# Kernel tuning notes

Measured on AMD Instinct MI355X. Metric: run time of the kernel, lower is better.

## Reference

```python
import jax, jax.numpy as jnp
import numpy as np

H = 128

def _rnn_layer(inp, W_ih, W_hh, b_ih, b_hh):
    # inp: [B, T, D]; precompute the input projection for all timesteps at once
    pre = jnp.einsum('btd,hd->bth', inp, W_ih) + b_ih + b_hh  # [B, T, H]
    B = inp.shape[0]
    h0 = jnp.zeros((B, H), dtype=inp.dtype)

    def step(h, p_t):  # p_t: [B, H]
        h_new = jnp.tanh(p_t + h @ W_hh.T)
        return h_new, h_new

    _, hs = jax.lax.scan(step, h0, jnp.swapaxes(pre, 0, 1))  # [T, B, H]
    return jnp.swapaxes(hs, 0, 1)  # [B, T, H]


def setup_inputs() -> dict:
    key = jax.random.key(0)
    ks = jax.random.split(key, 12)
    B, T, D = 64, 512, 2048
    s_in = 1.0 / np.sqrt(H)  # PyTorch RNN init scale ~ U(-1/sqrt(H), 1/sqrt(H))
    u = lambda k, shape: jax.random.uniform(k, shape, jnp.float32, -s_in, s_in)
    return {
        'x': jax.random.normal(ks[0], (B, T, D), jnp.float32),
        'W_ih1': u(ks[1], (H, D)),
        'W_hh1': u(ks[2], (H, H)),
        'b_ih1': u(ks[3], (H,)),
        'b_hh1': u(ks[4], (H,)),
        'W_ih2': u(ks[5], (H, H)),
        'W_hh2': u(ks[6], (H, H)),
        'b_ih2': u(ks[7], (H,)),
        'b_hh2': u(ks[8], (H,)),
        'W_fc': u(ks[9], (1, H)),
        'b_fc': u(ks[10], (1,)),
    }


def reference(x, W_ih1, W_hh1, b_ih1, b_hh1, W_ih2, W_hh2, b_ih2, b_hh2, W_fc, b_fc):
    h1 = _rnn_layer(x, W_ih1, W_hh1, b_ih1, b_hh1)   # [B, T, H]
    h2 = _rnn_layer(h1, W_ih2, W_hh2, b_ih2, b_hh2)  # [B, T, H]
    last = h2[:, -1, :]                               # [B, H]
    return last @ W_fc.T + b_fc                       # [B, 1]
```

## Files before the change

### kernel.cpp

```cpp
#include <hip/hip_runtime.h>
#include <cstddef>

#define BB 64
#define TT 512
#define DD 2048
#define HH 128
#define M1 (BB*TT)

__device__ __forceinline__ float tanh_fast(float x) {
    float e2x = __builtin_amdgcn_exp2f(x * 2.885390081777927f);
    return 1.0f - 2.0f * __builtin_amdgcn_rcpf(e2x + 1.0f);
}

template<int K>
__global__ __launch_bounds__(256) void gemm_bias_kernel(
    const float* __restrict__ A, const float* __restrict__ W,
    const float* __restrict__ bia, const float* __restrict__ bib,
    float* __restrict__ out)
{
    constexpr int BM = 64, BK = 16;
    constexpr int NK = K / BK;
    __shared__ float As[BK][68];
    __shared__ float Bs[BK][132];

    const int tid = threadIdx.x;
    const int tc = tid & 15;
    const int tr = tid >> 4;
    const size_t m0 = (size_t)blockIdx.x * BM;

    const int arow = tid >> 2;
    const int ak4  = (tid & 3) * 4;
    const int bn0  = tid >> 1;
    const int bk   = (tid & 1) * 8;

    const float* Aptr = A + (m0 + arow) * (size_t)K + ak4;
    const float* Wptr = W + (size_t)bn0 * K + bk;

    float4 ra  = *(const float4*)Aptr;
    float4 rb0 = *(const float4*)(Wptr);
    float4 rb1 = *(const float4*)(Wptr + 4);

    float acc[4][8];
#pragma unroll
    for (int i = 0; i < 4; i++)
#pragma unroll
        for (int j = 0; j < 8; j++) acc[i][j] = 0.0f;

    for (int kt = 0; kt < NK; ++kt) {
        __syncthreads();
        As[ak4 + 0][arow] = ra.x;
        As[ak4 + 1][arow] = ra.y;
        As[ak4 + 2][arow] = ra.z;
        As[ak4 + 3][arow] = ra.w;
        Bs[bk + 0][bn0] = rb0.x;
        Bs[bk + 1][bn0] = rb0.y;
        Bs[bk + 2][bn0] = rb0.z;
        Bs[bk + 3][bn0] = rb0.w;
        Bs[bk + 4][bn0] = rb1.x;
        Bs[bk + 5][bn0] = rb1.y;
        Bs[bk + 6][bn0] = rb1.z;
        Bs[bk + 7][bn0] = rb1.w;
        __syncthreads();
        if (kt + 1 < NK) {
            ra  = *(const float4*)(Aptr + (size_t)(kt + 1) * BK);
            rb0 = *(const float4*)(Wptr + (size_t)(kt + 1) * BK);
            rb1 = *(const float4*)(Wptr + (size_t)(kt + 1) * BK + 4);
        }
#pragma unroll
        for (int kk = 0; kk < BK; ++kk) {
            const float4 av = *(const float4*)&As[kk][tr * 4];
            const float4 b0 = *(const float4*)&Bs[kk][tc * 4];
            const float4 b1 = *(const float4*)&Bs[kk][64 + tc * 4];
            const float aa[4] = {av.x, av.y, av.z, av.w};
            const float bb[8] = {b0.x, b0.y, b0.z, b0.w, b1.x, b1.y, b1.z, b1.w};
#pragma unroll
            for (int i = 0; i < 4; i++)
#pragma unroll
                for (int j = 0; j < 8; j++)
                    acc[i][j] = __builtin_fmaf(aa[i], bb[j], acc[i][j]);
        }
    }

    float bs[8];
#pragma unroll
    for (int j = 0; j < 4; j++) {
        bs[j]     = bia[tc * 4 + j] + bib[tc * 4 + j];
        bs[j + 4] = bia[64 + tc * 4 + j] + bib[64 + tc * 4 + j];
    }
#pragma unroll
    for (int i = 0; i < 4; i++) {
        const size_t r = m0 + tr * 4 + i;
        float4 o0 = {acc[i][0] + bs[0], acc[i][1] + bs[1],
                     acc[i][2] + bs[2], acc[i][3] + bs[3]};
        float4 o1 = {acc[i][4] + bs[4], acc[i][5] + bs[5],
                     acc[i][6] + bs[6], acc[i][7] + bs[7]};
        *(float4*)&out[r * HH + tc * 4]      = o0;
        *(float4*)&out[r * HH + 64 + tc * 4] = o1;
    }
}

__global__ __launch_bounds__(512) void rnn_scan_kernel(
    const float* __restrict__ pre,
    const float* __restrict__ Whh,
    float* __restrict__ hout,
    const float* __restrict__ Wfc,
    const float* __restrict__ bfc,
    float* __restrict__ outv,
    const int store_h)
{
    __shared__ float hsh[2][160];
    __shared__ float wsum[8];

    const int tid  = threadIdx.x;
    const int wave = tid >> 6;
    const int lane = tid & 63;
    const int jj   = lane >> 3;
    const int kq   = lane & 7;
    const int j    = wave * 8 + jj;
    const int b    = blockIdx.x;


    float4 Wr0[4], Wr1[4];
    {
        const float* wp0 = Whh + (size_t)j * HH + kq * 16;
        const float* wp1 = Whh + (size_t)(j + 64) * HH + kq * 16;
#pragma unroll
        for (int q = 0; q < 4; q++) {
            Wr0[q] = *(const float4*)(wp0 + q * 4);
            Wr1[q] = *(const float4*)(wp1 + q * 4);
        }
    }

    if (tid < HH) hsh[0][(tid >> 4) * 20 + (tid & 15)] = 0.0f;
    __syncthreads();

    const float* pb = pre + (size_t)b * TT * HH;
    float pre_next0 = 0.f, pre_next1 = 0.f;
    if (kq == 0) { pre_next0 = pb[j]; pre_next1 = pb[j + 64]; }
    float hlast0 = 0.f, hlast1 = 0.f;

    for (int t = 0; t < TT; ++t) {
        const float* hr = hsh[t & 1];
        float* hw = hsh[(t + 1) & 1];
        const float pre_cur0 = pre_next0, pre_cur1 = pre_next1;
        if (kq == 0 && t + 1 < TT) {
            pre_next0 = pb[(size_t)(t + 1) * HH + j];
            pre_next1 = pb[(size_t)(t + 1) * HH + j + 64];
        }
        float acc0 = 0.f, acc1 = 0.f;
#pragma unroll
        for (int q = 0; q < 4; q++) {
            const float4 hv = *(const float4*)&hr[kq * 20 + q * 4];
            acc0 = __builtin_fmaf(Wr0[q].x, hv.x, acc0);
            acc0 = __builtin_fmaf(Wr0[q].y, hv.y, acc0);
            acc0 = __builtin_fmaf(Wr0[q].z, hv.z, acc0);
            acc0 = __builtin_fmaf(Wr0[q].w, hv.w, acc0);
            acc1 = __builtin_fmaf(Wr1[q].x, hv.x, acc1);
            acc1 = __builtin_fmaf(Wr1[q].y, hv.y, acc1);
            acc1 = __builtin_fmaf(Wr1[q].z, hv.z, acc1);
            acc1 = __builtin_fmaf(Wr1[q].w, hv.w, acc1);
        }
        acc0 += __shfl_xor(acc0, 1);  acc1 += __shfl_xor(acc1, 1);
        acc0 += __shfl_xor(acc0, 2);  acc1 += __shfl_xor(acc1, 2);
        acc0 += __shfl_xor(acc0, 4);  acc1 += __shfl_xor(acc1, 4);
        if (kq == 0) {
            const float h0 = tanh_fast(pre_cur0 + acc0);
            const float h1 = tanh_fast(pre_cur1 + acc1);
            hw[(j >> 4) * 20 + (j & 15)] = h0;
            hw[((j + 64) >> 4) * 20 + ((j + 64) & 15)] = h1;
            if (store_h) {
                hout[((size_t)b * TT + t) * HH + j]      = h0;
                hout[((size_t)b * TT + t) * HH + j + 64] = h1;
            }
            hlast0 = h0; hlast1 = h1;
        }
        __syncthreads();
    }

    if (!store_h) {
        float contrib = 0.f;
        if (kq == 0) contrib = hlast0 * Wfc[j] + hlast1 * Wfc[j + 64];
#pragma unroll
        for (int off = 1; off < 64; off <<= 1) contrib += __shfl_xor(contrib, off);
        if (lane == 0) wsum[wave] = contrib;
        __syncthreads();
        if (tid == 0) {
            float s = bfc[0];
#pragma unroll
            for (int w = 0; w < 8; w++) s += wsum[w];
            outv[b] = s;
        }
    }
}

extern "C" void kernel_launch(void* const* d_in, const int* in_sizes, int n_in,
                              void* d_out, int out_size, void* d_ws, size_t ws_size,
                              hipStream_t stream) {
    const float* x    = (const float*)d_in[0];
    const float* Wih1 = (const float*)d_in[1];
    const float* Whh1 = (const float*)d_in[2];
    const float* bih1 = (const float*)d_in[3];
    const float* bhh1 = (const float*)d_in[4];
    const float* Wih2 = (const float*)d_in[5];
    const float* Whh2 = (const float*)d_in[6];
    const float* bih2 = (const float*)d_in[7];
    const float* bhh2 = (const float*)d_in[8];
    const float* Wfc  = (const float*)d_in[9];
    const float* bfc  = (const float*)d_in[10];
    float* out = (float*)d_out;

    float* preA = (float*)d_ws;
    float* h1b  = preA + (size_t)M1 * HH;

    gemm_bias_kernel<DD><<<dim3(M1 / 64), dim3(256), 0, stream>>>(x, Wih1, bih1, bhh1, preA);
    rnn_scan_kernel<<<dim3(BB), dim3(512), 0, stream>>>(preA, Whh1, h1b, Wfc, bfc, out, 1);
    gemm_bias_kernel<HH><<<dim3(M1 / 64), dim3(256), 0, stream>>>(h1b, Wih2, bih2, bhh2, preA);
    rnn_scan_kernel<<<dim3(BB), dim3(512), 0, stream>>>(preA, Whh2, h1b, Wfc, bfc, out, 0);
}
```

Baseline: 940.5 us.

## Use f16 MFMA for input projections and f16 dot2 recurrent scan

Replaces the fp32 SIMT GEMMs with f16 MFMA 16x16x32 GEMMs, adding kernels that pre-convert the input weights to half precision. The recurrence scan drops from 512 to 128 threads, with each thread holding a full W_hh row in registers as packed halves and using fdot2, so the shuffle reduction goes away. The scan also prefetches 8 timesteps of pre-activations, and the hidden states passed to layer 2 are stored as f16 to halve that traffic. This targets both the GEMM compute cost and the per-step latency of the serial scan, at the cost of reduced precision.

```diff
diff --git a/kernel.cpp b/kernel.cpp
--- a/kernel.cpp
+++ b/kernel.cpp
@@ -1,5 +1,6 @@
 #include <hip/hip_runtime.h>
 #include <cstddef>
+#include <cstdint>
 
 #define BB 64
 #define TT 512
@@ -7,189 +8,171 @@
 #define HH 128
 #define M1 (BB*TT)
 
+typedef __attribute__((ext_vector_type(8))) _Float16 f16x8;
+typedef __attribute__((ext_vector_type(4))) float f32x4;
+typedef __attribute__((ext_vector_type(2))) _Float16 h2f;
+
 __device__ __forceinline__ float tanh_fast(float x) {
     float e2x = __builtin_amdgcn_exp2f(x * 2.885390081777927f);
     return 1.0f - 2.0f * __builtin_amdgcn_rcpf(e2x + 1.0f);
 }
-
-template<int K>
-__global__ __launch_bounds__(256) void gemm_bias_kernel(
-    const float* __restrict__ A, const float* __restrict__ W,
+__device__ __forceinline__ h2f bch2(unsigned u) { return __builtin_bit_cast(h2f, u); }
+
+__global__ __launch_bounds__(256) void prep_f16_kernel(
+    const float* __restrict__ W, _Float16* __restrict__ Wf)
+{
+    const int i = (blockIdx.x * 256 + threadIdx.x) * 4;
+    float4 w = *(const float4*)(W + i);
+    f16x8 dummy;
+    _Float16 o0 = (_Float16)w.x, o1 = (_Float16)w.y;
+    _Float16 o2 = (_Float16)w.z, o3 = (_Float16)w.w;
+    ushort4 ov;
+    ov.x = __builtin_bit_cast(unsigned short, o0);
+    ov.y = __builtin_bit_cast(unsigned short, o1);
+    ov.z = __builtin_bit_cast(unsigned short, o2);
+    ov.w = __builtin_bit_cast(unsigned short, o3);
+    *(ushort4*)((unsigned short*)Wf + i) = ov;
+    (void)dummy;
+}
+
+template<int K, bool CONVA>
+__global__ __launch_bounds__(256) void gemm_f16_mfma(
+    const void* __restrict__ Araw, const _Float16* __restrict__ Wf,
     const float* __restrict__ bia, const float* __restrict__ bib,
     float* __restrict__ out)
 {
-    constexpr int BM = 64, BK = 16;
-    constexpr int NK = K / BK;
-    __shared__ float As[BK][68];
-    __shared__ float Bs[BK][132];
-
-    const int tid = threadIdx.x;
-    const int tc = tid & 15;
-    const int tr = tid >> 4;
-    const size_t m0 = (size_t)blockIdx.x * BM;
-
-    const int arow = tid >> 2;
-    const int ak4  = (tid & 3) * 4;
-    const int bn0  = tid >> 1;
-    const int bk   = (tid & 1) * 8;
-
-    const float* Aptr = A + (m0 + arow) * (size_t)K + ak4;
-    const float* Wptr = W + (size_t)bn0 * K + bk;
-
-    float4 ra  = *(const float4*)Aptr;
-    float4 rb0 = *(const float4*)(Wptr);
-    float4 rb1 = *(const float4*)(Wptr + 4);
-
-    float acc[4][8];
-#pragma unroll
-    for (int i = 0; i < 4; i++)
-#pragma unroll
-        for (int j = 0; j < 8; j++) acc[i][j] = 0.0f;
+    constexpr int BK = 32, NK = K / BK;
+    __shared__ __align__(16) _Float16 Af[64 * 40];
+    __shared__ __align__(16) _Float16 Ws[128 * 40];
+
+    const int tid = threadIdx.x, wave = tid >> 6, lane = tid & 63;
+    const size_t m0 = (size_t)blockIdx.x * 64;
+    const int ar = tid >> 2, ak = (tid & 3) * 8;
+    const int wr = tid >> 1, wk = (tid & 1) * 16;
+    const _Float16* Wp = Wf + (size_t)wr * K + wk;
+    const int frow = lane & 15, fko = (lane >> 4) * 8;
+
+    f32x4 acc[8];
+#pragma unroll
+    for (int i = 0; i < 8; i++) acc[i] = (f32x4){0.f, 0.f, 0.f, 0.f};
 
     for (int kt = 0; kt < NK; ++kt) {
+        f16x8 astage;
+        if (CONVA) {
+            const float* Ap = (const float*)Araw + (m0 + ar) * (size_t)K + kt * BK + ak;
+            float4 a0 = *(const float4*)Ap;
+            float4 a1 = *(const float4*)(Ap + 4);
+            astage[0] = (_Float16)a0.x; astage[1] = (_Float16)a0.y;
+            astage[2] = (_Float16)a0.z; astage[3] = (_Float16)a0.w;
+            astage[4] = (_Float16)a1.x; astage[5] = (_Float16)a1.y;
+            astage[6] = (_Float16)a1.z; astage[7] = (_Float16)a1.w;
+        } else {
+            const _Float16* Ap = (const _Float16*)Araw + (m0 + ar) * (size_t)K + kt * BK + ak;
+            astage = *(const f16x8*)Ap;
+        }
+        f16x8 w0 = *(const f16x8*)(Wp + kt * BK);
+        f16x8 w1 = *(const f16x8*)(Wp + kt * BK + 8);
         __syncthreads();
-        As[ak4 + 0][arow] = ra.x;
-        As[ak4 + 1][arow] = ra.y;
-        As[ak4 + 2][arow] = ra.z;
-        As[ak4 + 3][arow] = ra.w;
-        Bs[bk + 0][bn0] = rb0.x;
-        Bs[bk + 1][bn0] = rb0.y;
-        Bs[bk + 2][bn0] = rb0.z;
-        Bs[bk + 3][bn0] = rb0.w;
-        Bs[bk + 4][bn0] = rb1.x;
-        Bs[bk + 5][bn0] = rb1.y;
-        Bs[bk + 6][bn0] = rb1.z;
-        Bs[bk + 7][bn0] = rb1.w;
+        *(f16x8*)&Af[ar * 40 + ak] = astage;
+        *(f16x8*)&Ws[wr * 40 + wk] = w0;
+        *(f16x8*)&Ws[wr * 40 + wk + 8] = w1;
         __syncthreads();
-        if (kt + 1 < NK) {
-            ra  = *(const float4*)(Aptr + (size_t)(kt + 1) * BK);
-            rb0 = *(const float4*)(Wptr + (size_t)(kt + 1) * BK);
-            rb1 = *(const float4*)(Wptr + (size_t)(kt + 1) * BK + 4);
-        }
-#pragma unroll
-        for (int kk = 0; kk < BK; ++kk) {
-            const float4 av = *(const float4*)&As[kk][tr * 4];
-            const float4 b0 = *(const float4*)&Bs[kk][tc * 4];
-            const float4 b1 = *(const float4*)&Bs[kk][64 + tc * 4];
-            const float aa[4] = {av.x, av.y, av.z, av.w};
-            const float bb[8] = {b0.x, b0.y, b0.z, b0.w, b1.x, b1.y, b1.z, b1.w};
-#pragma unroll
-            for (int i = 0; i < 4; i++)
-#pragma unroll
-                for (int j = 0; j < 8; j++)
-                    acc[i][j] = __builtin_fmaf(aa[i], bb[j], acc[i][j]);
-        }
-    }
-
-    float bs[8];
-#pragma unroll
-    for (int j = 0; j < 4; j++) {
-        bs[j]     = bia[tc * 4 + j] + bib[tc * 4 + j];
-        bs[j + 4] = bia[64 + tc * 4 + j] + bib[64 + tc * 4 + j];
-    }
-#pragma unroll
-    for (int i = 0; i < 4; i++) {
-        const size_t r = m0 + tr * 4 + i;
-        float4 o0 = {acc[i][0] + bs[0], acc[i][1] + bs[1],
-                     acc[i][2] + bs[2], acc[i][3] + bs[3]};
-        float4 o1 = {acc[i][4] + bs[4], acc[i][5] + bs[5],
-                     acc[i][6] + bs[6], acc[i][7] + bs[7]};
-        *(float4*)&out[r * HH + tc * 4]      = o0;
-        *(float4*)&out[r * HH + 64 + tc * 4] = o1;
-    }
-}
-
-__global__ __launch_bounds__(512) void rnn_scan_kernel(
+        f16x8 fA = *(const f16x8*)&Af[(wave * 16 + frow) * 40 + fko];
+#pragma unroll
+        for (int nt = 0; nt < 8; ++nt) {
+            f16x8 fW = *(const f16x8*)&Ws[(nt * 16 + frow) * 40 + fko];
+            acc[nt] = __builtin_amdgcn_mfma_f32_16x16x32_f16(fA, fW, acc[nt], 0, 0, 0);
+        }
+    }
+    const int rbase = (lane >> 4) * 4;
+#pragma unroll
+    for (int nt = 0; nt < 8; ++nt) {
+        const int col = nt * 16 + frow;
+        const float bv = bia[col] + bib[col];
+#pragma unroll
+        for (int r = 0; r < 4; r++)
+            out[(m0 + wave * 16 + rbase + r) * HH + col] = acc[nt][r] + bv;
+    }
+}
+
+template<bool STORE>
+__global__ __launch_bounds__(128) void rnn_scan2w(
     const float* __restrict__ pre,
     const float* __restrict__ Whh,
-    float* __restrict__ hout,
-    const float* __restrict__ Wfc,
-    const float* __restrict__ bfc,
-    float* __restrict__ outv,
-    const int store_h)
+    _Float16* __restrict__ hout,
+    const float* __restrict__ Wfc, const float* __restrict__ bfc,
+    float* __restrict__ outv)
 {
-    __shared__ float hsh[2][160];
-    __shared__ float wsum[8];
-
-    const int tid  = threadIdx.x;
-    const int wave = tid >> 6;
-    const int lane = tid & 63;
-    const int jj   = lane >> 3;
-    const int kq   = lane & 7;
-    const int j    = wave * 8 + jj;
-    const int b    = blockIdx.x;
-
-
-    float4 Wr0[4], Wr1[4];
+    __shared__ __align__(16) _Float16 hbuf[2][HH];
+    __shared__ float wsum[2];
+    const int tid = threadIdx.x;
+    const int w = tid >> 6, lane = tid & 63;
+    const int j = tid;
+    const int b = blockIdx.x;
+
+    h2f Wr[64];
     {
-        const float* wp0 = Whh + (size_t)j * HH + kq * 16;
-        const float* wp1 = Whh + (size_t)(j + 64) * HH + kq * 16;
-#pragma unroll
-        for (int q = 0; q < 4; q++) {
-            Wr0[q] = *(const float4*)(wp0 + q * 4);
-            Wr1[q] = *(const float4*)(wp1 + q * 4);
-        }
-    }
-
-    if (tid < HH) hsh[0][(tid >> 4) * 20 + (tid & 15)] = 0.0f;
+        const float* wp = Whh + (size_t)j * HH;
+#pragma unroll
+        for (int q = 0; q < 32; q++) {
+            float4 wv = *(const float4*)(wp + q * 4);
+            Wr[2 * q]     = h2f{(_Float16)wv.x, (_Float16)wv.y};
+            Wr[2 * q + 1] = h2f{(_Float16)wv.z, (_Float16)wv.w};
+        }
+    }
+    if (tid < 64) ((unsigned*)hbuf[0])[tid] = 0u;
     __syncthreads();
 
     const float* pb = pre + (size_t)b * TT * HH;
-    float pre_next0 = 0.f, pre_next1 = 0.f;
-    if (kq == 0) { pre_next0 = pb[j]; pre_next1 = pb[j + 64]; }
-    float hlast0 = 0.f, hlast1 = 0.f;
-
-    for (int t = 0; t < TT; ++t) {
-        const float* hr = hsh[t & 1];
-        float* hw = hsh[(t + 1) & 1];
-        const float pre_cur0 = pre_next0, pre_cur1 = pre_next1;
-        if (kq == 0 && t + 1 < TT) {
-            pre_next0 = pb[(size_t)(t + 1) * HH + j];
-            pre_next1 = pb[(size_t)(t + 1) * HH + j + 64];
-        }
-        float acc0 = 0.f, acc1 = 0.f;
-#pragma unroll
-        for (int q = 0; q < 4; q++) {
-            const float4 hv = *(const float4*)&hr[kq * 20 + q * 4];
-            acc0 = __builtin_fmaf(Wr0[q].x, hv.x, acc0);
-            acc0 = __builtin_fmaf(Wr0[q].y, hv.y, acc0);
-            acc0 = __builtin_fmaf(Wr0[q].z, hv.z, acc0);
-            acc0 = __builtin_fmaf(Wr0[q].w, hv.w, acc0);
-            acc1 = __builtin_fmaf(Wr1[q].x, hv.x, acc1);
-            acc1 = __builtin_fmaf(Wr1[q].y, hv.y, acc1);
-            acc1 = __builtin_fmaf(Wr1[q].z, hv.z, acc1);
-            acc1 = __builtin_fmaf(Wr1[q].w, hv.w, acc1);
-        }
-        acc0 += __shfl_xor(acc0, 1);  acc1 += __shfl_xor(acc1, 1);
-        acc0 += __shfl_xor(acc0, 2);  acc1 += __shfl_xor(acc1, 2);
-        acc0 += __shfl_xor(acc0, 4);  acc1 += __shfl_xor(acc1, 4);
-        if (kq == 0) {
-            const float h0 = tanh_fast(pre_cur0 + acc0);
-            const float h1 = tanh_fast(pre_cur1 + acc1);
-            hw[(j >> 4) * 20 + (j & 15)] = h0;
-            hw[((j + 64) >> 4) * 20 + ((j + 64) & 15)] = h1;
-            if (store_h) {
-                hout[((size_t)b * TT + t) * HH + j]      = h0;
-                hout[((size_t)b * TT + t) * HH + j + 64] = h1;
+    _Float16* hob = hout + (size_t)b * TT * HH;
+    float fc = 0.f;
+
+    constexpr int PF = 8;
+    float pf[PF];
+#pragma unroll
+    for (int i = 0; i < PF; i++) pf[i] = pb[(size_t)i * HH + j];
+
+    for (int tb = 0; tb < TT; tb += PF) {
+        const bool more = (tb + PF < TT);
+#pragma unroll
+        for (int u = 0; u < PF; u++) {
+            const int t = tb + u;
+            const float p = pf[u];
+            if (more) pf[u] = pb[(size_t)(t + PF) * HH + j];
+
+            const _Float16* hr = hbuf[t & 1];
+            _Float16* hw = hbuf[(t + 1) & 1];
+
+            float a[8];
+#pragma unroll
+            for (int q = 0; q < 8; q++) a[q] = 0.f;
+#pragma unroll
+            for (int q = 0; q < 16; q++) {
+                uint4 hv = *(const uint4*)&hr[q * 8];
+                float aq = a[q % 8];
+                aq = __builtin_amdgcn_fdot2(Wr[4 * q + 0], bch2(hv.x), aq, false);
+                aq = __builtin_amdgcn_fdot2(Wr[4 * q + 1], bch2(hv.y), aq, false);
+                aq = __builtin_amdgcn_fdot2(Wr[4 * q + 2], bch2(hv.z), aq, false);
+                aq = __builtin_amdgcn_fdot2(Wr[4 * q + 3], bch2(hv.w), aq, false);
+                a[q % 8] = aq;
             }
-            hlast0 = h0; hlast1 = h1;
-        }
+            const float s = (((a[0] + a[1]) + (a[2] + a[3])) +
+                             ((a[4] + a[5]) + (a[6] + a[7]))) + p;
+            const float h = tanh_fast(s);
+            const _Float16 hh = (_Float16)h;
+            hw[j] = hh;
+            if (STORE) hob[(size_t)t * HH + j] = hh;
+            if (t == TT - 1) fc = h * Wfc[j];
+            __syncthreads();
+        }
+    }
+
+    if (!STORE) {
+#pragma unroll
+        for (int off = 1; off < 64; off <<= 1) fc += __shfl_xor(fc, off);
+        if (lane == 0) wsum[w] = fc;
         __syncthreads();
-    }
-
-    if (!store_h) {
-        float contrib = 0.f;
-        if (kq == 0) contrib = hlast0 * Wfc[j] + hlast1 * Wfc[j + 64];
-#pragma unroll
-        for (int off = 1; off < 64; off <<= 1) contrib += __shfl_xor(contrib, off);
-        if (lane == 0) wsum[wave] = contrib;
-        __syncthreads();
-        if (tid == 0) {
-            float s = bfc[0];
-#pragma unroll
-            for (int w = 0; w < 8; w++) s += wsum[w];
-            outv[b] = s;
-        }
+        if (tid == 0) outv[b] = wsum[0] + wsum[1] + bfc[0];
     }
 }
 
@@ -209,11 +192,20 @@
     const float* bfc  = (const float*)d_in[10];
     float* out = (float*)d_out;
 
-    float* preA = (float*)d_ws;
-    float* h1b  = preA + (size_t)M1 * HH;
-
-    gemm_bias_kernel<DD><<<dim3(M1 / 64), dim3(256), 0, stream>>>(x, Wih1, bih1, bhh1, preA);
-    rnn_scan_kernel<<<dim3(BB), dim3(512), 0, stream>>>(preA, Whh1, h1b, Wfc, bfc, out, 1);
-    gemm_bias_kernel<HH><<<dim3(M1 / 64), dim3(256), 0, stream>>>(h1b, Wih2, bih2, bhh2, preA);
-    rnn_scan_kernel<<<dim3(BB), dim3(512), 0, stream>>>(preA, Whh2, h1b, Wfc, bfc, out, 0);
-}
+    char* wsp = (char*)d_ws;
+    float*     preA = (float*)wsp;
+    _Float16*  h1b  = (_Float16*)(wsp + (size_t)16 * 1024 * 1024);
+    _Float16*  W1f  = (_Float16*)(wsp + (size_t)24 * 1024 * 1024);
+    _Float16*  W2f  = (_Float16*)(wsp + (size_t)24 * 1024 * 1024 + 512 * 1024);
+
+    prep_f16_kernel<<<dim3(HH * DD / 1024), dim3(256), 0, stream>>>(Wih1, W1f);
+    prep_f16_kernel<<<dim3(HH * HH / 1024), dim3(256), 0, stream>>>(Wih2, W2f);
+    gemm_f16_mfma<DD, true><<<dim3(M1 / 64), dim3(256), 0, stream>>>(
+        x, W1f, bih1, bhh1, preA);
+    rnn_scan2w<true><<<dim3(BB), dim3(128), 0, stream>>>(
+        preA, Whh1, h1b, Wfc, bfc, out);
+    gemm_f16_mfma<HH, false><<<dim3(M1 / 64), dim3(256), 0, stream>>>(
+        h1b, W2f, bih2, bhh2, preA);
+    rnn_scan2w<false><<<dim3(BB), dim3(128), 0, stream>>>(
+        preA, Whh2, h1b, Wfc, bfc, out);
+}
```

New measurement: 1.043 ms. 1.11x slower.
